# Kernel tuning notes

Hardware: AMD Instinct MI355X
Metric: run time of the kernel (lower is better)

The kernel has to match this reference:

```python
import jax, jax.numpy as jnp
import numpy as np

EPSILON = 1e-05
LOG_2PI = float(np.log(2.0 * np.pi))


def setup_inputs() -> dict:
    key = jax.random.key(0)
    k1, k2, k3 = jax.random.split(key, 3)
    B, S, K, N = 64, 1000, 12, 80  # batch, seq, n_states, n_channels
    x = jax.random.normal(k1, (B, S, N), dtype=jnp.float32)
    mu = jax.random.normal(k2, (B, K, N), dtype=jnp.float32)
    # Positive-definite covariances per (batch, state)
    A = jax.random.normal(k3, (B, K, N, N), dtype=jnp.float32)
    sigma = A @ jnp.swapaxes(A, -1, -2) / N + jnp.eye(N, dtype=jnp.float32)
    return {"x": x, "mu": mu, "sigma": sigma}


def reference(x, mu, sigma):
    """Batched-over-states MVN log-likelihood.

    x: (B, S, N); mu: (B, K, N); sigma: (B, K, N, N).
    Returns log_likelihood: (B, S, K).
    """
    N = x.shape[-1]
    # add_epsilon with diag=True: epsilon * I on the diagonal
    sigma = sigma + jnp.asarray(EPSILON, sigma.dtype) * jnp.eye(N, dtype=sigma.dtype)
    L = jnp.linalg.cholesky(sigma)  # (B, K, N, N), batched across states
    diff = x[:, :, None, :] - mu[:, None, :, :]  # (B, S, K, N)
    # Solve L z = diff, batched: L -> (B, 1, K, N, N), diff -> (B, S, K, N, 1)
    z = jax.scipy.linalg.solve_triangular(L[:, None], diff[..., None], lower=True)[..., 0]
    quad = jnp.sum(z * z, axis=-1)  # (B, S, K)
    logdet_half = jnp.sum(jnp.log(jnp.diagonal(L, axis1=-2, axis2=-1)), axis=-1)  # (B, K)
    ll = -0.5 * quad - logdet_half[:, None, :] - 0.5 * N * jnp.asarray(LOG_2PI, x.dtype)
    return ll  # (B, S, K)
```

## Files before the change

kernel.cpp:

```cpp
#include <hip/hip_runtime.h>

#define Bb 64
#define Ss 1000
#define Kk 12
#define Nn 80
#define CTERM 73.51508265637381f
#define STA 84

typedef __attribute__((ext_vector_type(8))) short short8;
typedef __attribute__((ext_vector_type(4))) float f32x4;

static __device__ __forceinline__ unsigned short f2bf(float f) {
    unsigned u = __builtin_bit_cast(unsigned, f);
    unsigned r = u + 0x7FFFu + ((u >> 16) & 1u);
    return (unsigned short)(r >> 16);
}
static __device__ __forceinline__ float bf2f(unsigned short h) {
    unsigned u = ((unsigned)h) << 16;
    return __builtin_bit_cast(float, u);
}

__global__ __launch_bounds__(256, 3) void prep_kernel(
    const float* __restrict__ sigma, const float* __restrict__ mu,
    const float* __restrict__ x,
    uint4* __restrict__ wsWh, uint4* __restrict__ wsWl,
    float* __restrict__ wsV, float* __restrict__ wsL,
    uint4* __restrict__ Xh, uint4* __restrict__ Xl, int doX)
{
    __shared__ float Ls[Nn * STA];
    __shared__ float LT[Nn * Nn];
    __shared__ float invd[Nn];
    __shared__ float mus[Nn];

    const int bk  = blockIdx.x;
    const int tid = threadIdx.x;
    const int w   = tid >> 6;
    const int l   = tid & 63;
    const int r2  = l + 64;

    const float4* sp4 = (const float4*)(sigma + (size_t)bk * Nn * Nn);
    #pragma unroll
    for (int it = 0; it < 7; ++it) {
        int ci = tid + 256 * it;
        if (ci < 1600) {
            float4 v = sp4[ci];
            int r = ci / 20, c4 = 4 * (ci - 20 * r);
            *(float4*)&Ls[r * STA + c4] = v;
        }
    }
    if (tid < Nn) mus[tid] = mu[(size_t)bk * Nn + tid];
    __syncthreads();
    if (tid < Nn) Ls[tid * STA + tid] += 1e-5f;
    __syncthreads();

    float ldacc = 0.0f;
    for (int p = 0; p < 20; ++p) {
        const int j0 = 4 * p;
        const bool a1 = (l >= j0);
        const bool a2 = (l < 16) && (r2 >= j0);

        if (w == 0) {
            float B00 = Ls[j0*STA+j0];
            float B10 = Ls[(j0+1)*STA+j0], B11 = Ls[(j0+1)*STA+j0+1];
            float B20 = Ls[(j0+2)*STA+j0], B21 = Ls[(j0+2)*STA+j0+1], B22 = Ls[(j0+2)*STA+j0+2];
            float B30 = Ls[(j0+3)*STA+j0], B31 = Ls[(j0+3)*STA+j0+1], B32 = Ls[(j0+3)*STA+j0+2], B33 = Ls[(j0+3)*STA+j0+3];
            float rv0 = rsqrtf(B00);
            float l10 = B10*rv0, l20 = B20*rv0, l30 = B30*rv0;
            float t11 = fmaf(-l10,l10,B11);                    float rv1 = rsqrtf(t11);
            float l21 = fmaf(-l20,l10,B21)*rv1;
            float l31 = fmaf(-l30,l10,B31)*rv1;
            float t22 = fmaf(-l21,l21,fmaf(-l20,l20,B22));     float rv2 = rsqrtf(t22);
            float l32 = fmaf(-l31,l21,fmaf(-l30,l20,B32))*rv2;
            float t33 = fmaf(-l32,l32,fmaf(-l31,l31,fmaf(-l30,l30,B33)));
            float rv3 = rsqrtf(t33);
            ldacc += 0.5f * (logf(B00) + logf(t11) + logf(t22) + logf(t33));
            if (tid == 0) { invd[j0]=rv0; invd[j0+1]=rv1; invd[j0+2]=rv2; invd[j0+3]=rv3; }

            float b0=0.f,b1=0.f,b2=0.f,b3=0.f, c0=0.f,c1=0.f,c2=0.f,c3=0.f;
            if (a1) {
                float4 a = *(float4*)&Ls[l * STA + j0];
                b0 = a.x * rv0;
                b1 = fmaf(-l10, b0, a.y) * rv1;
                b2 = fmaf(-l21, b1, fmaf(-l20, b0, a.z)) * rv2;
                b3 = fmaf(-l32, b2, fmaf(-l31, b1, fmaf(-l30, b0, a.w))) * rv3;
                *(float4*)&Ls[l * STA + j0] = make_float4(b0, b1, b2, b3);
            }
            if (a2) {
                float4 a = *(float4*)&Ls[r2 * STA + j0];
                c0 = a.x * rv0;
                c1 = fmaf(-l10, c0, a.y) * rv1;
                c2 = fmaf(-l21, c1, fmaf(-l20, c0, a.z)) * rv2;
                c3 = fmaf(-l32, c2, fmaf(-l31, c1, fmaf(-l30, c0, a.w))) * rv3;
                *(float4*)&Ls[r2 * STA + j0] = make_float4(c0, c1, c2, c3);
            }
            LT[ j0   *Nn + l] = (l  > j0  ) ? b0 : 0.f;
            LT[(j0+1)*Nn + l] = (l  > j0+1) ? b1 : 0.f;
            LT[(j0+2)*Nn + l] = (l  > j0+2) ? b2 : 0.f;
            LT[(j0+3)*Nn + l] = (l  > j0+3) ? b3 : 0.f;
            if (l < 16) {
                LT[ j0   *Nn + r2] = (r2 > j0  ) ? c0 : 0.f;
                LT[(j0+1)*Nn + r2] = (r2 > j0+1) ? c1 : 0.f;
                LT[(j0+2)*Nn + r2] = (r2 > j0+2) ? c2 : 0.f;
                LT[(j0+3)*Nn + r2] = (r2 > j0+3) ? c3 : 0.f;
            }
        }
        __syncthreads();

        float4 bv = make_float4(0.f,0.f,0.f,0.f), cv = make_float4(0.f,0.f,0.f,0.f);
        if (a1) bv = *(float4*)&Ls[l * STA + j0];
        if (a2) cv = *(float4*)&Ls[r2 * STA + j0];
        #pragma unroll 2
        for (int g = p + 1 + w; g < 20; g += 4) {
            float4 u0 = *(const float4*)&LT[ j0   *Nn + 4*g];
            float4 u1 = *(const float4*)&LT[(j0+1)*Nn + 4*g];
            float4 u2 = *(const float4*)&LT[(j0+2)*Nn + 4*g];
            float4 u3 = *(const float4*)&LT[(j0+3)*Nn + 4*g];
            if (a1) {
                float4 t = *(float4*)&Ls[l * STA + 4*g];
                t.x = fmaf(-bv.x,u0.x, fmaf(-bv.y,u1.x, fmaf(-bv.z,u2.x, fmaf(-bv.w,u3.x, t.x))));
                t.y = fmaf(-bv.x,u0.y, fmaf(-bv.y,u1.y, fmaf(-bv.z,u2.y, fmaf(-bv.w,u3.y, t.y))));
                t.z = fmaf(-bv.x,u0.z, fmaf(-bv.y,u1.z, fmaf(-bv.z,u2.z, fmaf(-bv.w,u3.z, t.z))));
                t.w = fmaf(-bv.x,u0.w, fmaf(-bv.y,u1.w, fmaf(-bv.z,u2.w, fmaf(-bv.w,u3.w, t.w))));
                *(float4*)&Ls[l * STA + 4*g] = t;
            }
            if (a2) {
                float4 t = *(float4*)&Ls[r2 * STA + 4*g];
                t.x = fmaf(-cv.x,u0.x, fmaf(-cv.y,u1.x, fmaf(-cv.z,u2.x, fmaf(-cv.w,u3.x, t.x))));
                t.y = fmaf(-cv.x,u0.y, fmaf(-cv.y,u1.y, fmaf(-cv.z,u2.y, fmaf(-cv.w,u3.y, t.y))));
                t.z = fmaf(-cv.x,u0.z, fmaf(-cv.y,u1.z, fmaf(-cv.z,u2.z, fmaf(-cv.w,u3.z, t.z))));
                t.w = fmaf(-cv.x,u0.w, fmaf(-cv.y,u1.w, fmaf(-cv.z,u2.w, fmaf(-cv.w,u3.w, t.w))));
                *(float4*)&Ls[r2 * STA + 4*g] = t;
            }
        }
        __syncthreads();
    }
    if (tid == 0) wsL[bk] = ldacc;

    if (tid < Nn) {
        #pragma unroll
        for (int g = 0; g < 20; ++g)
            *(float4*)&Ls[tid * STA + 4*g] = make_float4(0.f, 0.f, 0.f, 0.f);
        Ls[tid * STA + tid] = 1.0f;
    }
    __syncthreads();

    for (int p = 0; p < 20; ++p) {
        const int i0 = 4 * p;
        const bool b1a = (i0 + 3 >= l);
        const bool b2a = (l < 16) && (i0 + 3 >= r2);

        if (w == 0) {
            float m10 = LT[ i0   *Nn + i0+1];
            float m20 = LT[ i0   *Nn + i0+2];
            float m30 = LT[ i0   *Nn + i0+3];
            float m21 = LT[(i0+1)*Nn + i0+2];
            float m31 = LT[(i0+1)*Nn + i0+3];
            float m32 = LT[(i0+2)*Nn + i0+3];
            float4 iv = *(const float4*)&invd[i0];
            if (b1a) {
                float4 a = *(float4*)&Ls[l * STA + i0];
                float w0 = a.x * iv.x;
                float w1 = fmaf(-w0, m10, a.y) * iv.y;
                float w2 = fmaf(-w1, m21, fmaf(-w0, m20, a.z)) * iv.z;
                float w3 = fmaf(-w2, m32, fmaf(-w1, m31, fmaf(-w0, m30, a.w))) * iv.w;
                *(float4*)&Ls[l * STA + i0] = make_float4(w0, w1, w2, w3);
            }
            if (b2a) {
                float4 a = *(float4*)&Ls[r2 * STA + i0];
                float v0 = a.x * iv.x;
                float v1 = fmaf(-v0, m10, a.y) * iv.y;
                float v2 = fmaf(-v1, m21, fmaf(-v0, m20, a.z)) * iv.z;
                float v3 = fmaf(-v2, m32, fmaf(-v1, m31, fmaf(-v0, m30, a.w))) * iv.w;
                *(float4*)&Ls[r2 * STA + i0] = make_float4(v0, v1, v2, v3);
            }
        }
        __syncthreads();

        float4 wv = make_float4(0.f,0.f,0.f,0.f), vv = make_float4(0.f,0.f,0.f,0.f);
        if (b1a) wv = *(float4*)&Ls[l * STA + i0];
        if (b2a) vv = *(float4*)&Ls[r2 * STA + i0];
        if (b1a | b2a) {
            #pragma unroll 2
            for (int g = p + 1 + w; g < 20; g += 4) {
                float4 u0 = *(const float4*)&LT[ i0   *Nn + 4*g];
                float4 u1 = *(const float4*)&LT[(i0+1)*Nn + 4*g];
                float4 u2 = *(const float4*)&LT[(i0+2)*Nn + 4*g];
                float4 u3 = *(const float4*)&LT[(i0+3)*Nn + 4*g];
                if (b1a) {
                    float4 t = *(float4*)&Ls[l * STA + 4*g];
                    t.x = fmaf(-wv.x,u0.x, fmaf(-wv.y,u1.x, fmaf(-wv.z,u2.x, fmaf(-wv.w,u3.x, t.x))));
                    t.y = fmaf(-wv.x,u0.y, fmaf(-wv.y,u1.y, fmaf(-wv.z,u2.y, fmaf(-wv.w,u3.y, t.y))));
                    t.z = fmaf(-wv.x,u0.z, fmaf(-wv.y,u1.z, fmaf(-wv.z,u2.z, fmaf(-wv.w,u3.z, t.z))));
                    t.w = fmaf(-wv.x,u0.w, fmaf(-wv.y,u1.w, fmaf(-wv.z,u2.w, fmaf(-wv.w,u3.w, t.w))));
                    *(float4*)&Ls[l * STA + 4*g] = t;
                }
                if (b2a) {
                    float4 t = *(float4*)&Ls[r2 * STA + 4*g];
                    t.x = fmaf(-vv.x,u0.x, fmaf(-vv.y,u1.x, fmaf(-vv.z,u2.x, fmaf(-vv.w,u3.x, t.x))));
                    t.y = fmaf(-vv.x,u0.y, fmaf(-vv.y,u1.y, fmaf(-vv.z,u2.y, fmaf(-vv.w,u3.y, t.y))));
                    t.z = fmaf(-vv.x,u0.z, fmaf(-vv.y,u1.z, fmaf(-vv.z,u2.z, fmaf(-vv.w,u3.z, t.z))));
                    t.w = fmaf(-vv.x,u0.w, fmaf(-vv.y,u1.w, fmaf(-vv.z,u2.w, fmaf(-vv.w,u3.w, t.w))));
                    *(float4*)&Ls[r2 * STA + 4*g] = t;
                }
            }
        }
        __syncthreads();
    }

    {
        float* vpart = LT;
        float s1 = 0.f, s2 = 0.f;
        const int c0 = 20 * w;
        #pragma unroll 4
        for (int cc = 0; cc < 20; ++cc) {
            int c = c0 + cc;
            float mc = mus[c];
            s1 = fmaf(Ls[c * STA + l], mc, s1);
            if (l < 16) s2 = fmaf(Ls[c * STA + r2], mc, s2);
        }
        vpart[w * Nn + l] = s1;
        if (l < 16) vpart[w * Nn + r2] = s2;
        __syncthreads();
        if (tid < Nn)
            wsV[(size_t)bk * Nn + tid] =
                vpart[tid] + vpart[Nn + tid] + vpart[2*Nn + tid] + vpart[3*Nn + tid];
    }
    const int n = l & 15, quad = l >> 4;
    uint4* ph = wsWh + (size_t)bk * 800;
    uint4* pq = wsWl + (size_t)bk * 800;
    for (int f = w; f < 10; f += 4) {
        int ks = f / 5, mt = f - 5 * ks;
        int m = 16 * mt + n, kb = 32 * ks + 8 * quad;
        unsigned hh[8], lo[8];
        #pragma unroll
        for (int j = 0; j < 8; ++j) {
            float wj = Ls[(kb + j) * STA + m];
            unsigned short h = f2bf(wj);
            hh[j] = h; lo[j] = f2bf(wj - bf2f(h));
        }
        ph[f*64 + l] = make_uint4(hh[0]|(hh[1]<<16), hh[2]|(hh[3]<<16), hh[4]|(hh[5]<<16), hh[6]|(hh[7]<<16));
        pq[f*64 + l] = make_uint4(lo[0]|(lo[1]<<16), lo[2]|(lo[3]<<16), lo[4]|(lo[5]<<16), lo[6]|(lo[7]<<16));
    }
    for (int mt = w; mt < 5; mt += 4) {
        if (quad < 2) {
            int m = 16 * mt + n, kb = 64 + 8 * quad;
            unsigned hh[8], lo[8];
            #pragma unroll
            for (int j = 0; j < 8; ++j) {
                float wj = Ls[(kb + j) * STA + m];
                unsigned short h = f2bf(wj);
                hh[j] = h; lo[j] = f2bf(wj - bf2f(h));
            }
            ph[640 + mt*32 + l] = make_uint4(hh[0]|(hh[1]<<16), hh[2]|(hh[3]<<16), hh[4]|(hh[5]<<16), hh[6]|(hh[7]<<16));
            pq[640 + mt*32 + l] = make_uint4(lo[0]|(lo[1]<<16), lo[2]|(lo[3]<<16), lo[4]|(lo[5]<<16), lo[6]|(lo[7]<<16));
        }
    }

    if (doX) {
        const int wid = bk * 4 + w;
        for (int it = 0; ; ++it) {
            int grp = wid + 3072 * it;
            if (grp >= 10000) break;
            int gcid = grp * 64 + l;
            int b2  = gcid / 10000;
            int rem = gcid - b2 * 10000;
            int s   = rem / 10, ch = rem - 10 * s;
            int k0  = 8 * ch;
            const float* xp = x + ((size_t)b2 * Ss + s) * Nn + k0;
            float4 f0 = *(const float4*)xp;
            float4 f1 = *(const float4*)(xp + 4);
            float d[8] = {f0.x, f0.y, f0.z, f0.w, f1.x, f1.y, f1.z, f1.w};
            unsigned hh[8], lo[8];
            #pragma unroll
            for (int j = 0; j < 8; ++j) {
                unsigned short h = f2bf(d[j]);
                hh[j] = h; lo[j] = f2bf(d[j] - bf2f(h));
            }
            int ks = k0 >> 5, qd = (k0 >> 3) & 3;
            size_t slot = ((size_t)(b2 * 64 + (s >> 4)) * 3 + ks) * 64 + qd * 16 + (s & 15);
            Xh[slot] = make_uint4(hh[0]|(hh[1]<<16), hh[2]|(hh[3]<<16), hh[4]|(hh[5]<<16), hh[6]|(hh[7]<<16));
            Xl[slot] = make_uint4(lo[0]|(lo[1]<<16), lo[2]|(lo[3]<<16), lo[4]|(lo[5]<<16), lo[6]|(lo[7]<<16));
        }
    }
}

__global__ __launch_bounds__(256) void ll_kernel2(
    const uint4* __restrict__ Xh, const uint4* __restrict__ Xl,
    const uint4* __restrict__ wsWh, const uint4* __restrict__ wsWl,
    const float* __restrict__ wsV, const float* __restrict__ wsL,
    float* __restrict__ out)
{
    __shared__ uint4 WhL[960], WlL[960];
    const int b = blockIdx.x;
    const int k = blockIdx.y;
    const int bk = b * Kk + k;
    const int tid = threadIdx.x;
    const int wv = tid >> 6, lane = tid & 63;
    const int n = lane & 15, quad = lane >> 4;

    const uint4* gh = wsWh + (size_t)bk * 800;
    const uint4* gl = wsWl + (size_t)bk * 800;
    #pragma unroll
    for (int it = 0; it < 3; ++it) {
        int i = tid + 256 * it;
        if (i < 640) { WhL[i] = gh[i]; WlL[i] = gl[i]; }
    }
    #pragma unroll
    for (int it = 0; it < 2; ++it) {
        int i = tid + 256 * it;
        if (i < 320) {
            int mt = i >> 6, ln = i & 63, qd = (ln >> 4);
            uint4 vh = make_uint4(0,0,0,0), vl = make_uint4(0,0,0,0);
            if (qd < 2) { vh = gh[640 + mt*32 + ln]; vl = gl[640 + mt*32 + ln]; }
            WhL[640 + i] = vh; WlL[640 + i] = vl;
        }
    }
    __syncthreads();

    const float ld = wsL[bk];
    f32x4 vf[5];
    #pragma unroll
    for (int mt = 0; mt < 5; ++mt)
        vf[mt] = *(const f32x4*)&wsV[(size_t)bk * Nn + 16*mt + 4*quad];

    for (int st = 0; st < 8; ++st) {
        const int sg0 = st * 8 + wv * 2;
        short8 bh[2][3], bl[2][3];
        #pragma unroll
        for (int t = 0; t < 2; ++t)
            #pragma unroll
            for (int ks = 0; ks < 3; ++ks) {
                size_t base = ((size_t)(b * 64 + sg0 + t) * 3 + ks) * 64 + lane;
                bh[t][ks] = __builtin_bit_cast(short8, Xh[base]);
                bl[t][ks] = __builtin_bit_cast(short8, Xl[base]);
            }

        f32x4 acc[2][5];
        #pragma unroll
        for (int t = 0; t < 2; ++t)
            #pragma unroll
            for (int mt = 0; mt < 5; ++mt) acc[t][mt] = (f32x4){0.f,0.f,0.f,0.f};

        #pragma unroll
        for (int ks = 0; ks < 3; ++ks) {
            #pragma unroll
            for (int mt = 0; mt < 5; ++mt) {
                const int fi = (ks < 2) ? (ks*5 + mt)*64 + lane : 640 + mt*64 + lane;
                short8 wh = __builtin_bit_cast(short8, WhL[fi]);
                short8 wl = __builtin_bit_cast(short8, WlL[fi]);
                #pragma unroll
                for (int t = 0; t < 2; ++t) {
                    acc[t][mt] = __builtin_amdgcn_mfma_f32_16x16x32_bf16(wh, bh[t][ks], acc[t][mt], 0, 0, 0);
                    acc[t][mt] = __builtin_amdgcn_mfma_f32_16x16x32_bf16(wl, bh[t][ks], acc[t][mt], 0, 0, 0);
                    acc[t][mt] = __builtin_amdgcn_mfma_f32_16x16x32_bf16(wh, bl[t][ks], acc[t][mt], 0, 0, 0);
                }
            }
        }

        #pragma unroll
        for (int t = 0; t < 2; ++t) {
            float q2 = 0.f;
            #pragma unroll
            for (int mt = 0; mt < 5; ++mt)
                #pragma unroll
                for (int r = 0; r < 4; ++r) {
                    float y = acc[t][mt][r] - vf[mt][r];
                    q2 = fmaf(y, y, q2);
                }
            q2 += __shfl_xor(q2, 16, 64);
            q2 += __shfl_xor(q2, 32, 64);
            int gs = st * 128 + wv * 32 + 16 * t + n;
            if (lane < 16 && gs < Ss)
                out[((size_t)b * Ss + gs) * Kk + k] = -0.5f * q2 - ld - CTERM;
        }
    }
}

__global__ __launch_bounds__(256) void ll_kernel(
    const float* __restrict__ x,
    const uint4* __restrict__ wsWh, const uint4* __restrict__ wsWl,
    const float* __restrict__ wsV, const float* __restrict__ wsL,
    float* __restrict__ out)
{
    const int b    = blockIdx.x;
    const int st   = blockIdx.y;
    const int tid  = threadIdx.x;
    const int wv   = tid >> 6, lane = tid & 63;
    const int n    = lane & 15, quad = lane >> 4;
    const int sbase = st * 128 + wv * 32;

    short8 xh[2][3], xl[2][3];
    #pragma unroll
    for (int t = 0; t < 2; ++t) {
        int gs = sbase + 16 * t + n;
        #pragma unroll
        for (int ks = 0; ks < 3; ++ks) {
            int kb = 32 * ks + 8 * quad;
            float d[8] = {0.f,0.f,0.f,0.f,0.f,0.f,0.f,0.f};
            if (gs < Ss && kb < Nn) {
                const float* xp = x + ((size_t)b * Ss + gs) * Nn + kb;
                float4 f0 = *(const float4*)xp;
                float4 f1 = *(const float4*)(xp + 4);
                d[0]=f0.x; d[1]=f0.y; d[2]=f0.z; d[3]=f0.w;
                d[4]=f1.x; d[5]=f1.y; d[6]=f1.z; d[7]=f1.w;
            }
            short8 h, lo2;
            #pragma unroll
            for (int j = 0; j < 8; ++j) {
                unsigned short hv = f2bf(d[j]);
                h[j]   = (short)hv;
                lo2[j] = (short)f2bf(d[j] - bf2f(hv));
            }
            xh[t][ks] = h; xl[t][ks] = lo2;
        }
    }

    for (int k = 0; k < Kk; ++k) {
        const int bk = b * Kk + k;
        const uint4* ah_p = wsWh + (size_t)bk * 800;
        const uint4* al_p = wsWl + (size_t)bk * 800;

        f32x4 acc[2][5];
        #pragma unroll
        for (int t = 0; t < 2; ++t)
            #pragma unroll
            for (int mt = 0; mt < 5; ++mt) acc[t][mt] = (f32x4){0.f,0.f,0.f,0.f};

        #pragma unroll
        for (int ks = 0; ks < 3; ++ks) {
            short8 ah[5], al[5];
            if (ks < 2) {
                #pragma unroll
                for (int mt = 0; mt < 5; ++mt) {
                    ah[mt] = __builtin_bit_cast(short8, ah_p[(ks*5 + mt)*64 + lane]);
                    al[mt] = __builtin_bit_cast(short8, al_p[(ks*5 + mt)*64 + lane]);
                }
            } else {
                #pragma unroll
                for (int mt = 0; mt < 5; ++mt) {
                    uint4 zh = make_uint4(0,0,0,0), zl = make_uint4(0,0,0,0);
                    if (quad < 2) {
                        zh = ah_p[640 + mt*32 + lane];
                        zl = al_p[640 + mt*32 + lane];
                    }
                    ah[mt] = __builtin_bit_cast(short8, zh);
                    al[mt] = __builtin_bit_cast(short8, zl);
                }
            }
            #pragma unroll
            for (int mt = 0; mt < 5; ++mt)
                #pragma unroll
                for (int t = 0; t < 2; ++t) {
                    acc[t][mt] = __builtin_amdgcn_mfma_f32_16x16x32_bf16(ah[mt], xh[t][ks], acc[t][mt], 0, 0, 0);
                    acc[t][mt] = __builtin_amdgcn_mfma_f32_16x16x32_bf16(al[mt], xh[t][ks], acc[t][mt], 0, 0, 0);
                    acc[t][mt] = __builtin_amdgcn_mfma_f32_16x16x32_bf16(ah[mt], xl[t][ks], acc[t][mt], 0, 0, 0);
                }
        }

        float ld = wsL[bk];
        f32x4 vf[5];
        #pragma unroll
        for (int mt = 0; mt < 5; ++mt)
            vf[mt] = *(const f32x4*)&wsV[(size_t)bk * Nn + 16*mt + 4*quad];
        #pragma unroll
        for (int t = 0; t < 2; ++t) {
            float q2 = 0.f;
            #pragma unroll
            for (int mt = 0; mt < 5; ++mt)
                #pragma unroll
                for (int r = 0; r < 4; ++r) {
                    float y = acc[t][mt][r] - vf[mt][r];
                    q2 = fmaf(y, y, q2);
                }
            q2 += __shfl_xor(q2, 16, 64);
            q2 += __shfl_xor(q2, 32, 64);
            int gs = sbase + 16 * t + n;
            if (lane < 16 && gs < Ss)
                out[((size_t)b * Ss + gs) * Kk + k] = -0.5f * q2 - ld - CTERM;
        }
    }
}

#define ST1 81
__global__ __launch_bounds__(256) void mvn_ll_fallback(
    const float* __restrict__ x, const float* __restrict__ mu,
    const float* __restrict__ sigma, float* __restrict__ out)
{
    __shared__ float Ls[Nn * ST1];
    __shared__ float invd[Nn];
    __shared__ float mus[Nn];
    __shared__ float logdet_s;

    const int bk = blockIdx.x, b = bk / Kk, k = bk - b * Kk;
    const int tid = threadIdx.x, nt = blockDim.x;

    const float* sp = sigma + (size_t)bk * Nn * Nn;
    for (int t = tid; t < Nn * Nn; t += nt) Ls[(t / Nn) * ST1 + (t % Nn)] = sp[t];
    if (tid < Nn) mus[tid] = mu[(size_t)bk * Nn + tid];
    __syncthreads();
    if (tid < Nn) Ls[tid * ST1 + tid] += 1e-5f;
    __syncthreads();
    for (int j = 0; j < Nn; ++j) {
        if (tid == 0) {
            float d = sqrtf(Ls[j * ST1 + j]);
            Ls[j * ST1 + j] = d; invd[j] = 1.0f / d;
        }
        __syncthreads();
        const float inv = invd[j];
        for (int i = j + 1 + tid; i < Nn; i += nt) Ls[i * ST1 + j] *= inv;
        __syncthreads();
        for (int t = tid; t < Nn * Nn; t += nt) {
            int r = t / Nn, c = t % Nn;
            if (r > j && c > j && c <= r)
                Ls[r * ST1 + c] -= Ls[r * ST1 + j] * Ls[c * ST1 + j];
        }
        __syncthreads();
    }
    if (tid == 0) {
        float a = 0.f; for (int j = 0; j < Nn; ++j) a += logf(Ls[j * ST1 + j]);
        logdet_s = a;
    }
    __syncthreads();
    const float ld = logdet_s;
    for (int s = tid; s < Ss; s += nt) {
        const float4* xp = (const float4*)(x + ((size_t)b * Ss + s) * Nn);
        float a[Nn];
        #pragma unroll
        for (int q = 0; q < Nn / 4; ++q) {
            float4 v = xp[q];
            a[4*q+0] = v.x - mus[4*q+0]; a[4*q+1] = v.y - mus[4*q+1];
            a[4*q+2] = v.z - mus[4*q+2]; a[4*q+3] = v.w - mus[4*q+3];
        }
        #pragma unroll
        for (int i = 0; i < Nn; ++i) {
            float t = a[i];
            #pragma unroll
            for (int j = 0; j < i; ++j) t = fmaf(-Ls[i * ST1 + j], a[j], t);
            a[i] = t * invd[i];
        }
        float quad = 0.f;
        #pragma unroll
        for (int i = 0; i < Nn; ++i) quad = fmaf(a[i], a[i], quad);
        out[((size_t)b * Ss + s) * Kk + k] = -0.5f * quad - ld - CTERM;
    }
}

extern "C" void kernel_launch(void* const* d_in, const int* in_sizes, int n_in,
                              void* d_out, int out_size, void* d_ws, size_t ws_size,
                              hipStream_t stream) {
    const float* x     = (const float*)d_in[0];
    const float* mu    = (const float*)d_in[1];
    const float* sigma = (const float*)d_in[2];
    float* out = (float*)d_out;

    const size_t nBK   = (size_t)Bb * Kk;
    const size_t nWu4  = nBK * 800;
    const size_t nXu4  = (size_t)Bb * 64 * 3 * 64;
    const size_t need_mid  = nWu4 * 16 * 2 + nBK * Nn * 4 + nBK * 4;
    const size_t need_full = need_mid + nXu4 * 16 * 2;

    if (ws_size >= need_full) {
        uint4* wsWh = (uint4*)d_ws;
        uint4* wsWl = wsWh + nWu4;
        uint4* Xh   = wsWl + nWu4;
        uint4* Xl   = Xh + nXu4;
        float* wsV  = (float*)(Xl + nXu4);
        float* wsL  = wsV + nBK * Nn;
        prep_kernel<<<dim3(Bb * Kk), dim3(256), 0, stream>>>(
            sigma, mu, x, wsWh, wsWl, wsV, wsL, Xh, Xl, 1);
        ll_kernel2<<<dim3(Bb, Kk), dim3(256), 0, stream>>>(Xh, Xl, wsWh, wsWl, wsV, wsL, out);
    } else if (ws_size >= need_mid) {
        uint4* wsWh = (uint4*)d_ws;
        uint4* wsWl = wsWh + nWu4;
        float* wsV  = (float*)(wsWl + nWu4);
        float* wsL  = wsV + nBK * Nn;
        prep_kernel<<<dim3(Bb * Kk), dim3(256), 0, stream>>>(
            sigma, mu, x, wsWh, wsWl, wsV, wsL, (uint4*)nullptr, (uint4*)nullptr, 0);
        ll_kernel<<<dim3(Bb, 8), dim3(256), 0, stream>>>(x, wsWh, wsWl, wsV, wsL, out);
    } else {
        mvn_ll_fallback<<<dim3(Bb * Kk), dim3(256), 0, stream>>>(x, mu, sigma, out);
    }
}
```

Before: 166.8 us.

## Rotate Cholesky panel owner across waves, drop per-step barrier, remap X pack

The Cholesky factorisation and triangular inverse now rotate which wave factors each 4-column panel, chosen by p mod 4, instead of always using wave 0. Each wave's trailing-update column groups are remapped so it updates the group the next panel owner needs, which lets the code drop one __syncthreads per step. The log-determinant partials are now accumulated per wave and summed through shared memory. The X bf16 hi/lo packing is remapped so each wave writes 64 contiguous output slots (coalesced stores), with zero padding for rows past the sequence end. The risk is a subtle ordering dependency once the second barrier is gone.

```diff
diff --git a/kernel.cpp b/kernel.cpp
--- a/kernel.cpp
+++ b/kernel.cpp
@@ -31,6 +31,7 @@
     __shared__ float LT[Nn * Nn];
     __shared__ float invd[Nn];
     __shared__ float mus[Nn];
+    __shared__ float ldp[4];
 
     const int bk  = blockIdx.x;
     const int tid = threadIdx.x;
@@ -59,7 +60,7 @@
         const bool a1 = (l >= j0);
         const bool a2 = (l < 16) && (r2 >= j0);
 
-        if (w == 0) {
+        if (w == (p & 3)) {
             float B00 = Ls[j0*STA+j0];
             float B10 = Ls[(j0+1)*STA+j0], B11 = Ls[(j0+1)*STA+j0+1];
             float B20 = Ls[(j0+2)*STA+j0], B21 = Ls[(j0+2)*STA+j0+1], B22 = Ls[(j0+2)*STA+j0+2];
@@ -74,7 +75,7 @@
             float t33 = fmaf(-l32,l32,fmaf(-l31,l31,fmaf(-l30,l30,B33)));
             float rv3 = rsqrtf(t33);
             ldacc += 0.5f * (logf(B00) + logf(t11) + logf(t22) + logf(t33));
-            if (tid == 0) { invd[j0]=rv0; invd[j0+1]=rv1; invd[j0+2]=rv2; invd[j0+3]=rv3; }
+            if (l == 0) { invd[j0]=rv0; invd[j0+1]=rv1; invd[j0+2]=rv2; invd[j0+3]=rv3; }
 
             float b0=0.f,b1=0.f,b2=0.f,b3=0.f, c0=0.f,c1=0.f,c2=0.f,c3=0.f;
             if (a1) {
@@ -109,8 +110,10 @@
         float4 bv = make_float4(0.f,0.f,0.f,0.f), cv = make_float4(0.f,0.f,0.f,0.f);
         if (a1) bv = *(float4*)&Ls[l * STA + j0];
         if (a2) cv = *(float4*)&Ls[r2 * STA + j0];
+        const int gs0 = p + 1;
+        const int g0 = gs0 + ((w - gs0) & 3);
         #pragma unroll 2
-        for (int g = p + 1 + w; g < 20; g += 4) {
+        for (int g = g0; g < 20; g += 4) {
             float4 u0 = *(const float4*)&LT[ j0   *Nn + 4*g];
             float4 u1 = *(const float4*)&LT[(j0+1)*Nn + 4*g];
             float4 u2 = *(const float4*)&LT[(j0+2)*Nn + 4*g];
@@ -132,9 +135,10 @@
                 *(float4*)&Ls[r2 * STA + 4*g] = t;
             }
         }
-        __syncthreads();
-    }
-    if (tid == 0) wsL[bk] = ldacc;
+    }
+    if (l == 0) ldp[w] = ldacc;
+    __syncthreads();
+    if (tid == 0) wsL[bk] = ldp[0] + ldp[1] + ldp[2] + ldp[3];
 
     if (tid < Nn) {
         #pragma unroll
@@ -149,7 +153,7 @@
         const bool b1a = (i0 + 3 >= l);
         const bool b2a = (l < 16) && (i0 + 3 >= r2);
 
-        if (w == 0) {
+        if (w == (p & 3)) {
             float m10 = LT[ i0   *Nn + i0+1];
             float m20 = LT[ i0   *Nn + i0+2];
             float m30 = LT[ i0   *Nn + i0+3];
@@ -180,8 +184,10 @@
         if (b1a) wv = *(float4*)&Ls[l * STA + i0];
         if (b2a) vv = *(float4*)&Ls[r2 * STA + i0];
         if (b1a | b2a) {
+            const int gs0 = p + 1;
+            const int g0 = gs0 + ((w - gs0) & 3);
             #pragma unroll 2
-            for (int g = p + 1 + w; g < 20; g += 4) {
+            for (int g = g0; g < 20; g += 4) {
                 float4 u0 = *(const float4*)&LT[ i0   *Nn + 4*g];
                 float4 u1 = *(const float4*)&LT[(i0+1)*Nn + 4*g];
                 float4 u2 = *(const float4*)&LT[(i0+2)*Nn + 4*g];
@@ -204,8 +210,8 @@
                 }
             }
         }
-        __syncthreads();
-    }
+    }
+    __syncthreads();
 
     {
         float* vpart = LT;
@@ -258,26 +264,31 @@
 
     if (doX) {
         const int wid = bk * 4 + w;
-        for (int it = 0; ; ++it) {
-            int grp = wid + 3072 * it;
-            if (grp >= 10000) break;
-            int gcid = grp * 64 + l;
-            int b2  = gcid / 10000;
-            int rem = gcid - b2 * 10000;
-            int s   = rem / 10, ch = rem - 10 * s;
-            int k0  = 8 * ch;
-            const float* xp = x + ((size_t)b2 * Ss + s) * Nn + k0;
-            float4 f0 = *(const float4*)xp;
-            float4 f1 = *(const float4*)(xp + 4);
-            float d[8] = {f0.x, f0.y, f0.z, f0.w, f1.x, f1.y, f1.z, f1.w};
+        const int qd = l >> 4, n2 = l & 15;
+        #pragma unroll
+        for (int it = 0; it < 4; ++it) {
+            int G = wid + 3072 * it;
+            if (G >= 12096) break;
+            int b2  = G / 189;
+            int rem = G - b2 * 189;
+            int sg  = rem / 3, ks = rem - 3 * sg;
+            int s   = sg * 16 + n2;
+            int k0  = 32 * ks + 8 * qd;
+            float d[8] = {0.f,0.f,0.f,0.f,0.f,0.f,0.f,0.f};
+            if (s < Ss) {
+                const float* xp = x + ((size_t)b2 * Ss + s) * Nn + k0;
+                float4 f0 = *(const float4*)xp;
+                float4 f1 = *(const float4*)(xp + 4);
+                d[0]=f0.x; d[1]=f0.y; d[2]=f0.z; d[3]=f0.w;
+                d[4]=f1.x; d[5]=f1.y; d[6]=f1.z; d[7]=f1.w;
+            }
             unsigned hh[8], lo[8];
             #pragma unroll
             for (int j = 0; j < 8; ++j) {
                 unsigned short h = f2bf(d[j]);
                 hh[j] = h; lo[j] = f2bf(d[j] - bf2f(h));
             }
-            int ks = k0 >> 5, qd = (k0 >> 3) & 3;
-            size_t slot = ((size_t)(b2 * 64 + (s >> 4)) * 3 + ks) * 64 + qd * 16 + (s & 15);
+            size_t slot = ((size_t)(b2 * 64 + sg) * 3 + ks) * 64 + l;
             Xh[slot] = make_uint4(hh[0]|(hh[1]<<16), hh[2]|(hh[3]<<16), hh[4]|(hh[5]<<16), hh[6]|(hh[7]<<16));
             Xl[slot] = make_uint4(lo[0]|(lo[1]<<16), lo[2]|(lo[3]<<16), lo[4]|(lo[5]<<16), lo[6]|(lo[7]<<16));
         }
```

Result: no change. 168.1 us (+0.8%).
